# Performance work log

Measured on AMD Instinct MI355X. Metric: run time of the kernel, lower is better.

The kernel has to match this reference:

```python
import jax, jax.numpy as jnp
import numpy as np

B, T, C, H = 2, 2048, 1024, 16
NS, NL, STEP = 3, 1, 8            # n_s_token, n_l_token, online_step
NPF = NS + NL                      # tokens per frame
CHUNK = STEP * NPF                 # online chunk size = 32
D = C // H


def _build_causal_mask():
    # Faithful port of the buffer construction in __init__ (host-side numpy).
    m = np.tril(np.ones((T, T), dtype=np.float32))
    step = np.zeros((T, T), dtype=np.float32)
    for i in range(0, T, CHUNK):
        step[i:i + CHUNK, i:i + CHUNK] = 1.0
        for j in range(i, i + CHUNK, NPF):
            m[j + NS:j + NPF, :] = 0.0
            m[:, j + NS:j + NPF] = 0.0
    return jnp.asarray(((m + step) == 0.0))[None, None]  # (1,1,T,T) bool


def setup_inputs() -> dict:
    key = jax.random.key(0)
    ks = jax.random.split(key, 10)
    sc = 0.02
    return {
        "x": jax.random.normal(ks[0], (B, T, C), dtype=jnp.float32),
        "dynamic_mask": jax.random.randint(ks[1], (B, 1, T, T), 0, 2).astype(bool),
        "causal_mask": _build_causal_mask(),
        "Wq": jax.random.normal(ks[2], (C, C), dtype=jnp.float32) * sc,
        "bq": jnp.zeros((C,), dtype=jnp.float32),
        "Wk": jax.random.normal(ks[3], (C, C), dtype=jnp.float32) * sc,
        "bk": jnp.zeros((C,), dtype=jnp.float32),
        "Wv": jax.random.normal(ks[4], (C, C), dtype=jnp.float32) * sc,
        "bv": jnp.zeros((C,), dtype=jnp.float32),
        "Wo": jax.random.normal(ks[5], (C, C), dtype=jnp.float32) * sc,
        "bo": jnp.zeros((C,), dtype=jnp.float32),
    }


def reference(x, dynamic_mask, causal_mask, Wq, bq, Wk, bk, Wv, bv, Wo, bo):
    Bb, Tt, Cc = x.shape
    scale = jnp.asarray(D, x.dtype) ** -0.5
    # nn.Linear: y = x @ W.T + b ; split heads -> (B,H,T,D)
    q = (x @ Wq.T + bq).reshape(Bb, Tt, H, D).transpose(0, 2, 1, 3)
    k = (x @ Wk.T + bk).reshape(Bb, Tt, H, D).transpose(0, 2, 1, 3)
    v = (x @ Wv.T + bv).reshape(Bb, Tt, H, D).transpose(0, 2, 1, 3)
    att = jnp.einsum('bhqd,bhkd->bhqk', q, k) * scale       # (B,H,T,T)
    neg_inf = jnp.asarray(-jnp.inf, att.dtype)
    att = jnp.where(causal_mask, neg_inf, att)
    att = jnp.where(dynamic_mask, neg_inf, att)
    att = jax.nn.softmax(att, axis=-1)                      # attn_drop is identity (eval)
    y = jnp.einsum('bhqk,bhkd->bhqd', att, v)
    y = y.transpose(0, 2, 1, 3).reshape(Bb, Tt, Cc)
    return y @ Wo.T + bo                                    # resid_drop is identity (eval)
```

## Files before the change

kernel.cpp:

```cpp
#include <hip/hip_runtime.h>

#define TSEQ 2048
#define NHEAD 16
#define DHEAD 64
#define CDIM 1024
#define BATCH 2

typedef __attribute__((ext_vector_type(8))) short bfx8;
typedef __attribute__((ext_vector_type(4))) short bfx4;
typedef __attribute__((ext_vector_type(4))) float f32x4;

__device__ __forceinline__ unsigned short f2bf(float f) {
  unsigned u = __builtin_bit_cast(unsigned, f);
  u += 0x7fffu + ((u >> 16) & 1u);
  return (unsigned short)(u >> 16);
}

__device__ __forceinline__ unsigned cvtpk(float lo, float hi) {
  unsigned r;
  asm("v_cvt_pk_bf16_f32 %0, %1, %2" : "=v"(r) : "v"(lo), "v"(hi));
  return r;
}

__device__ __forceinline__ float max3f(float a, float b, float c) {
  float d;
  asm("v_max3_f32 %0, %1, %2, %3" : "=v"(d) : "v"(a), "v"(b), "v"(c));
  return d;
}

__device__ __forceinline__ void gload16(const void* g, void* l) {
  __builtin_amdgcn_global_load_lds(
      (const __attribute__((address_space(1))) unsigned*)g,
      (__attribute__((address_space(3))) unsigned*)l, 16, 0, 0);
}

__global__ __launch_bounds__(256) void convert_all(
    const float* __restrict__ x,
    const float* __restrict__ wq, const float* __restrict__ wk,
    const float* __restrict__ wv, const float* __restrict__ wo,
    short* __restrict__ xb, short* __restrict__ wall) {
  const int y = blockIdx.y;
  const float* src;
  short* dst;
  int n;
  if (y == 0) { src = x; dst = xb; n = (BATCH * TSEQ * CDIM) / 4; }
  else {
    src = (y == 1) ? wq : (y == 2) ? wk : (y == 3) ? wv : wo;
    dst = wall + (size_t)(y - 1) * CDIM * CDIM;
    n = (CDIM * CDIM) / 4;
  }
  const int i = blockIdx.x * 256 + threadIdx.x;
  if (i < n) {
    const float4 v = ((const float4*)src)[i];
    bfx4 o;
    o[0] = (short)f2bf(v.x); o[1] = (short)f2bf(v.y);
    o[2] = (short)f2bf(v.z); o[3] = (short)f2bf(v.w);
    ((bfx4*)dst)[i] = o;
  }
}

__global__ __launch_bounds__(256) void maskpack(
    const unsigned char* __restrict__ dyn,
    const unsigned char* __restrict__ causal,
    unsigned long long* __restrict__ pm) {
  const bool mbyte = (causal[32] != 0);
  const int wave = threadIdx.x >> 6, lane = threadIdx.x & 63;
  const int gid = blockIdx.x * 4 + wave;
  const int tile = gid & 31;
  const int q = (gid >> 5) & (TSEQ - 1);
  const int b = gid >> 16;
  const int g = lane >> 4, blk = (lane >> 2) & 3, r = lane & 3;
  const int k = tile * 64 + blk * 16 + g * 4 + r;
  const size_t off = ((size_t)b * TSEQ + q) * TSEQ + k;
  const bool dm = mbyte ? (dyn[off] != 0) : (((const int*)dyn)[off] != 0);
  const bool qok = (q & 3) != 3;
  const bool al =
      (((k >> 5) == (q >> 5)) || ((k <= q) && qok && (r != 3))) && !dm;
  const unsigned long long bal = __ballot(!al);
  if (lane == 0) pm[gid] = bal;
}

template <int MODE>
__global__ __launch_bounds__(256) void gemm_nt(
    const short* __restrict__ A, const short* __restrict__ Ball,
    const float* __restrict__ bias0, const float* __restrict__ bias1,
    const float* __restrict__ bias2,
    short* __restrict__ Oq, short* __restrict__ Ok, short* __restrict__ Ov,
    float* __restrict__ Of) {
  __shared__ char arena[34816];
  const int tid = threadIdx.x;
  const int w = tid >> 6, lane = tid & 63;
  const int lq = lane & 15, g = lane >> 4;
  const int wr = w >> 1, wc = w & 1;
  const int m0 = blockIdx.x * 128, n0 = blockIdx.y * 128;
  const int which = (MODE == 0) ? (int)blockIdx.z : 3;
  const short* B = Ball + (size_t)which * CDIM * CDIM;
#define ASB(bi) ((short*)(arena + (bi) * 8192))
#define BSB(bi) ((short*)(arena + 16384 + (bi) * 8192))
#define GS(bi, kt)                                                             \
  {                                                                            \
    _Pragma("unroll") for (int ph = 0; ph < 2; ++ph) {                         \
      const int c = ph * 256 + tid;                                            \
      gload16(A + (size_t)(m0 + (c >> 2)) * CDIM + (kt) * 32 + (c & 3) * 8,    \
              ASB(bi) + (ph * 256 + w * 64) * 8);                              \
      gload16(B + (size_t)(n0 + (c >> 2)) * CDIM + (kt) * 32 + (c & 3) * 8,    \
              BSB(bi) + (ph * 256 + w * 64) * 8);                              \
    }                                                                          \
  }
  GS(0, 0);
  __syncthreads();
  f32x4 acc[4][4] = {};
  for (int kt = 0; kt < CDIM / 32; ++kt) {
    const int bi = kt & 1;
    if (kt + 1 < CDIM / 32) GS(bi ^ 1, kt + 1);
    bfx8 af[4], bfr[4];
#pragma unroll
    for (int i = 0; i < 4; ++i)
      af[i] = *(const bfx8*)&ASB(bi)[(wr * 64 + i * 16 + lq) * 32 + g * 8];
#pragma unroll
    for (int i = 0; i < 4; ++i)
      bfr[i] = *(const bfx8*)&BSB(bi)[(wc * 64 + i * 16 + lq) * 32 + g * 8];
#pragma unroll
    for (int i = 0; i < 4; ++i)
#pragma unroll
      for (int j = 0; j < 4; ++j)
        acc[i][j] = __builtin_amdgcn_mfma_f32_16x16x32_bf16(af[i], bfr[j],
                                                            acc[i][j], 0, 0, 0);
    __syncthreads();
  }
#undef GS
  if (MODE == 0) {
    const float* bias = (which == 0) ? bias0 : (which == 1) ? bias1 : bias2;
    const float scale = (which == 0) ? 0.18033688011112042f : 1.0f;
    short* O = (which == 0) ? Oq : (which == 1) ? Ok : Ov;
    short* tile = (short*)arena;
#pragma unroll
    for (int i = 0; i < 4; ++i)
#pragma unroll
      for (int j = 0; j < 4; ++j) {
        const int col = wc * 64 + j * 16 + lq;
        const float bb = bias[n0 + col];
#pragma unroll
        for (int r = 0; r < 4; ++r) {
          const int row = wr * 64 + i * 16 + g * 4 + r;
          tile[row * 136 + col] = (short)f2bf((acc[i][j][r] + bb) * scale);
        }
      }
    __syncthreads();
#pragma unroll
    for (int it = 0; it < 8; ++it) {
      const int id = it * 256 + tid;
      const int m = id >> 4, c16 = id & 15;
      const int row = m0 + m;
      const int b_ = row >> 11, t = row & (TSEQ - 1);
      const int h = (n0 >> 6) + (c16 >> 3), d0 = (c16 & 7) * 8;
      *(bfx8*)&O[(((size_t)b_ * NHEAD + h) * TSEQ + t) * DHEAD + d0] =
          *(const bfx8*)&tile[m * 136 + c16 * 8];
    }
  } else {
    const float* bias = bias0;
#pragma unroll
    for (int i = 0; i < 4; ++i)
#pragma unroll
      for (int j = 0; j < 4; ++j) {
        const int col = n0 + wc * 64 + j * 16 + lq;
        const float bb = bias[col];
#pragma unroll
        for (int r = 0; r < 4; ++r) {
          const int row = m0 + wr * 64 + i * 16 + g * 4 + r;
          Of[(size_t)row * CDIM + col] = acc[i][j][r] + bb;
        }
      }
  }
}

__global__ __launch_bounds__(256) void vtrans(const short* __restrict__ V,
                                              short* __restrict__ VT) {
  __shared__ short tile[64][72];
  const int bh = blockIdx.y;
  const int t0 = blockIdx.x * 64;
  const int tid = threadIdx.x;
  const short* src = V + ((size_t)bh * TSEQ + t0) * DHEAD;
#pragma unroll
  for (int ph = 0; ph < 4; ++ph) {
    const int c = ph * 256 + tid;
    const int row = c >> 4, col = (c & 15) * 4;
    *(bfx4*)&tile[row][col] = *(const bfx4*)(src + row * DHEAD + col);
  }
  __syncthreads();
  short* dst = VT + (size_t)bh * DHEAD * TSEQ + t0;
#pragma unroll
  for (int ph = 0; ph < 4; ++ph) {
    const int c = ph * 256 + tid;
    const int d = c >> 4, tc = (c & 15) * 4;
    bfx4 o;
    o[0] = tile[tc][d]; o[1] = tile[tc + 1][d];
    o[2] = tile[tc + 2][d]; o[3] = tile[tc + 3][d];
    *(bfx4*)(dst + (size_t)d * TSEQ + tc) = o;
  }
}

struct QPhase {
  bfx8 qf0, qf1;
  f32x4 acc[4];
  float m, l;
  const unsigned short* pmr;
};

__device__ __forceinline__ void attn_half(QPhase& S, const char* kbuf,
                                          const char* vbuf, short* Pw, int t,
                                          int hf, int sw, int lq, int g) {
  const unsigned mb = (S.pmr[t << 2] >> (hf * 8)) & 0xffu;
  f32x4 st[2] = {};
  __builtin_amdgcn_s_setprio(1);
#pragma unroll
  for (int b2 = 0; b2 < 2; ++b2) {
    const int rowb = ((hf * 2 + b2) * 16 + lq) * 128;
    const bfx8 kf0 = *(const bfx8*)&kbuf[rowb + ((g * 16) ^ sw)];
    const bfx8 kf1 = *(const bfx8*)&kbuf[rowb + ((64 + g * 16) ^ sw)];
    st[b2] =
        __builtin_amdgcn_mfma_f32_16x16x32_bf16(kf0, S.qf0, st[b2], 0, 0, 0);
    st[b2] =
        __builtin_amdgcn_mfma_f32_16x16x32_bf16(kf1, S.qf1, st[b2], 0, 0, 0);
  }
  __builtin_amdgcn_s_setprio(0);
  float s8[8];
#pragma unroll
  for (int idx = 0; idx < 8; ++idx)
    s8[idx] = ((mb >> idx) & 1u) ? -3.0e38f : st[idx >> 2][idx & 3];
  const float t0 = max3f(s8[0], s8[1], s8[2]);
  const float t1 = max3f(s8[3], s8[4], s8[5]);
  const float pmax = max3f(t0, t1, fmaxf(s8[6], s8[7]));
  if (!__all(pmax - S.m <= 8.f)) {
    float smax = fmaxf(pmax, __shfl_xor(pmax, 16));
    smax = fmaxf(smax, __shfl_xor(smax, 32));
    const float mnew = fmaxf(S.m, smax);
    const float fac = __builtin_amdgcn_exp2f(S.m - mnew);
    S.l *= fac;
    float fr[4];
#pragma unroll
    for (int r = 0; r < 4; ++r) fr[r] = __shfl(fac, g * 4 + r);
#pragma unroll
    for (int dc = 0; dc < 4; ++dc) {
      S.acc[dc][0] *= fr[0]; S.acc[dc][1] *= fr[1];
      S.acc[dc][2] *= fr[2]; S.acc[dc][3] *= fr[3];
    }
    S.m = mnew;
  }
  float psum = 0.f;
#pragma unroll
  for (int idx = 0; idx < 8; ++idx) {
    const float e = __builtin_amdgcn_exp2f(s8[idx] - S.m);
    s8[idx] = e;
    psum += e;
  }
  S.l += psum;
#pragma unroll
  for (int b2 = 0; b2 < 2; ++b2) {
    uint2 u;
    u.x = cvtpk(s8[b2 * 4 + 0], s8[b2 * 4 + 1]);
    u.y = cvtpk(s8[b2 * 4 + 2], s8[b2 * 4 + 3]);
    *(uint2*)&Pw[lq * 40 + b2 * 16 + g * 4] = u;
  }
  __builtin_amdgcn_wave_barrier();
  const bfx8 pa = *(const bfx8*)&Pw[lq * 40 + g * 8];
  __builtin_amdgcn_wave_barrier();
  __builtin_amdgcn_s_setprio(1);
#pragma unroll
  for (int dc = 0; dc < 4; ++dc) {
    const bfx8 vf = *(const bfx8*)&vbuf[(dc * 16 + lq) * 128 +
                                        ((hf * 64 + g * 16) ^ sw)];
    S.acc[dc] =
        __builtin_amdgcn_mfma_f32_16x16x32_bf16(pa, vf, S.acc[dc], 0, 0, 0);
  }
  __builtin_amdgcn_s_setprio(0);
}

__global__ __launch_bounds__(512, 4) void attn(
    const short* __restrict__ Q, const short* __restrict__ K,
    const short* __restrict__ VT, const unsigned short* __restrict__ pm,
    short* __restrict__ Y) {
  __shared__ char arena[53248];
  const int tid = threadIdx.x;
  const int w = tid >> 6, lane = tid & 63;
  const int hf = w >> 2, ws = w & 3;
  const int lq = lane & 15, g = lane >> 4;
  const int bh = blockIdx.y, b = bh >> 4, h = bh & 15;
  const int tlo = blockIdx.x, thi = 31 - tlo;
  const short* Qb = Q + (size_t)bh * TSEQ * DHEAD;
  const short* Kb = K + (size_t)bh * TSEQ * DHEAD;
  const short* Vb = VT + (size_t)bh * DHEAD * TSEQ;

  QPhase lo, hi;
  {
    const int qlo = tlo * 64 + ws * 16 + lq;
    const int qhi = thi * 64 + ws * 16 + lq;
    lo.qf0 = *(const bfx8*)(Qb + (size_t)qlo * DHEAD + g * 8);
    lo.qf1 = *(const bfx8*)(Qb + (size_t)qlo * DHEAD + 32 + g * 8);
    hi.qf0 = *(const bfx8*)(Qb + (size_t)qhi * DHEAD + g * 8);
    hi.qf1 = *(const bfx8*)(Qb + (size_t)qhi * DHEAD + 32 + g * 8);
#pragma unroll
    for (int dc = 0; dc < 4; ++dc) { lo.acc[dc] = f32x4{}; hi.acc[dc] = f32x4{}; }
    lo.m = -1e30f; lo.l = 0.f; hi.m = -1e30f; hi.l = 0.f;
    lo.pmr = pm + ((size_t)(b * TSEQ + qlo) << 7) + g;
    hi.pmr = pm + ((size_t)(b * TSEQ + qhi) << 7) + g;
  }

  const int sl = lane >> 3, sc = lane & 7;
  const int ssw = (sc ^ sl) * 8;
  const int sw = (lq & 7) << 4;
  short* Pw = (short*)(arena + 32768 + w * 1280);
  short* P2w = (short*)(arena + 43008 + w * 1280);

#define STAGE(bufn, k0s)                                                      \
  {                                                                           \
    gload16(Kb + (size_t)((k0s) + w * 8 + sl) * DHEAD + ssw,                  \
            arena + (bufn) * 16384 + w * 1024);                               \
    gload16(Vb + (size_t)(w * 8 + sl) * TSEQ + (k0s) + ssw,                   \
            arena + (bufn) * 16384 + 8192 + w * 1024);                        \
  }

  STAGE(0, 0);
  __syncthreads();

  for (int t = 0; t <= thi; ++t) {
    const int buf = t & 1;
    if (t < thi) STAGE(buf ^ 1, (t + 1) * 64);
    const char* kbuf = arena + buf * 16384;
    const char* vbuf = kbuf + 8192;
    attn_half(hi, kbuf, vbuf, Pw, t, hf, sw, lq, g);
    if (t <= tlo) attn_half(lo, kbuf, vbuf, P2w, t, hf, sw, lq, g);
    __syncthreads();
  }
#undef STAGE

  float* exA = (float*)arena;
  float2* exM = (float2*)(arena + 32768);
  if (hf == 1) {
#pragma unroll
    for (int ph = 0; ph < 2; ++ph) {
      QPhase& S = ph ? hi : lo;
      float* a = exA + (ws * 2 + ph) * 1024;
#pragma unroll
      for (int dc = 0; dc < 4; ++dc)
        *(f32x4*)&a[lane * 16 + dc * 4] = S.acc[dc];
      exM[(ws * 2 + ph) * 64 + lane] = float2{S.m, S.l};
    }
  }
  __syncthreads();
  if (hf == 0) {
#pragma unroll
    for (int ph = 0; ph < 2; ++ph) {
      QPhase& S = ph ? hi : lo;
      const float* a = exA + (ws * 2 + ph) * 1024;
      const float2 mlB = exM[(ws * 2 + ph) * 64 + lane];
      const float ms = fmaxf(S.m, mlB.x);
      const float fA = __builtin_amdgcn_exp2f(S.m - ms);
      const float fB = __builtin_amdgcn_exp2f(mlB.x - ms);
      float lr = S.l * fA + mlB.y * fB;
      lr += __shfl_xor(lr, 16);
      lr += __shfl_xor(lr, 32);
      float frA[4], frB[4], li[4];
#pragma unroll
      for (int r = 0; r < 4; ++r) {
        frA[r] = __shfl(fA, g * 4 + r);
        frB[r] = __shfl(fB, g * 4 + r);
        const float lv = __shfl(lr, g * 4 + r);
        li[r] = lv > 0.f ? 1.f / lv : 0.f;
      }
      const int q0 = (ph ? thi : tlo) * 64 + ws * 16;
#pragma unroll
      for (int dc = 0; dc < 4; ++dc) {
        const f32x4 ab = *(const f32x4*)&a[lane * 16 + dc * 4];
#pragma unroll
        for (int r = 0; r < 4; ++r) {
          const int t = q0 + g * 4 + r;
          Y[((size_t)b * TSEQ + t) * CDIM + h * DHEAD + dc * 16 + lq] =
              (short)f2bf((S.acc[dc][r] * frA[r] + ab[r] * frB[r]) * li[r]);
        }
      }
    }
  }
}

extern "C" void kernel_launch(void* const* d_in, const int* in_sizes, int n_in,
                              void* d_out, int out_size, void* d_ws,
                              size_t ws_size, hipStream_t stream) {
  const float* x = (const float*)d_in[0];
  const unsigned char* dyn = (const unsigned char*)d_in[1];
  const unsigned char* causal = (const unsigned char*)d_in[2];
  const float* Wq = (const float*)d_in[3];
  const float* bq = (const float*)d_in[4];
  const float* Wk = (const float*)d_in[5];
  const float* bk = (const float*)d_in[6];
  const float* Wv = (const float*)d_in[7];
  const float* bv = (const float*)d_in[8];
  const float* Wo = (const float*)d_in[9];
  const float* bo = (const float*)d_in[10];

  char* ws = (char*)d_ws;
  const size_t MB8 = 8ull * 1024 * 1024;
  short* xb = (short*)(ws + 0 * MB8);
  short* wall = (short*)(ws + 1 * MB8);
  short* Qb = (short*)(ws + 2 * MB8);
  short* Kb = (short*)(ws + 3 * MB8);
  short* Vb = (short*)(ws + 4 * MB8);
  short* VTb = (short*)(ws + 5 * MB8);
  short* Yb = (short*)(ws + 6 * MB8);
  unsigned long long* pmask = (unsigned long long*)(ws + 7 * MB8);

  convert_all<<<dim3(4096, 5), 256, 0, stream>>>(x, Wq, Wk, Wv, Wo, xb, wall);
  maskpack<<<dim3(32768), 256, 0, stream>>>(dyn, causal, pmask);
  gemm_nt<0><<<dim3(32, 8, 3), 256, 0, stream>>>(xb, wall, bq, bk, bv, Qb, Kb,
                                                 Vb, nullptr);
  vtrans<<<dim3(32, 32), 256, 0, stream>>>(Vb, VTb);
  attn<<<dim3(16, 32), 512, 0, stream>>>(Qb, Kb, VTb,
                                         (const unsigned short*)pmask, Yb);
  gemm_nt<1><<<dim3(32, 8, 1), 256, 0, stream>>>(Yb, wall, bo, nullptr, nullptr,
                                                 nullptr, nullptr, nullptr,
                                                 (float*)d_out);
}
```

Baseline: 137.9 us.

## Fuse V transpose into QKV GEMM, retile output GEMM, share attention P buffer

The QKV projection epilogue now writes V directly in transposed layout through a padded LDS tile, which removes the separate vtrans kernel launch and its read/write pass over V. The output projection becomes its own kernel with 64-row tiles, doubling the grid to 512 blocks to fill more CUs. The attention kernel reuses one P scratch buffer for both query halves, cutting LDS use and possibly allowing more resident blocks. Risks include bank conflicts in the strided transpose reads and a hazard on the shared P buffer between the two halves.

```diff
diff --git a/kernel.cpp b/kernel.cpp
--- a/kernel.cpp
+++ b/kernel.cpp
@@ -80,20 +80,18 @@
   if (lane == 0) pm[gid] = bal;
 }
 
-template <int MODE>
-__global__ __launch_bounds__(256) void gemm_nt(
+__global__ __launch_bounds__(256) void gemm_qkv(
     const short* __restrict__ A, const short* __restrict__ Ball,
     const float* __restrict__ bias0, const float* __restrict__ bias1,
     const float* __restrict__ bias2,
-    short* __restrict__ Oq, short* __restrict__ Ok, short* __restrict__ Ov,
-    float* __restrict__ Of) {
-  __shared__ char arena[34816];
+    short* __restrict__ Oq, short* __restrict__ Ok, short* __restrict__ VT) {
+  __shared__ char arena[35072];
   const int tid = threadIdx.x;
   const int w = tid >> 6, lane = tid & 63;
   const int lq = lane & 15, g = lane >> 4;
   const int wr = w >> 1, wc = w & 1;
   const int m0 = blockIdx.x * 128, n0 = blockIdx.y * 128;
-  const int which = (MODE == 0) ? (int)blockIdx.z : 3;
+  const int which = blockIdx.z;
   const short* B = Ball + (size_t)which * CDIM * CDIM;
 #define ASB(bi) ((short*)(arena + (bi) * 8192))
 #define BSB(bi) ((short*)(arena + 16384 + (bi) * 8192))
@@ -129,75 +127,106 @@
     __syncthreads();
   }
 #undef GS
-  if (MODE == 0) {
-    const float* bias = (which == 0) ? bias0 : (which == 1) ? bias1 : bias2;
-    const float scale = (which == 0) ? 0.18033688011112042f : 1.0f;
-    short* O = (which == 0) ? Oq : (which == 1) ? Ok : Ov;
-    short* tile = (short*)arena;
-#pragma unroll
-    for (int i = 0; i < 4; ++i)
-#pragma unroll
-      for (int j = 0; j < 4; ++j) {
-        const int col = wc * 64 + j * 16 + lq;
-        const float bb = bias[n0 + col];
-#pragma unroll
-        for (int r = 0; r < 4; ++r) {
-          const int row = wr * 64 + i * 16 + g * 4 + r;
-          tile[row * 136 + col] = (short)f2bf((acc[i][j][r] + bb) * scale);
-        }
+  const float* bias = (which == 0) ? bias0 : (which == 1) ? bias1 : bias2;
+  const float scale = (which == 0) ? 0.18033688011112042f : 1.0f;
+  short* tile = (short*)arena;
+  const int rs = (which == 2) ? 137 : 136;
+#pragma unroll
+  for (int i = 0; i < 4; ++i)
+#pragma unroll
+    for (int j = 0; j < 4; ++j) {
+      const int col = wc * 64 + j * 16 + lq;
+      const float bb = bias[n0 + col];
+#pragma unroll
+      for (int r = 0; r < 4; ++r) {
+        const int row = wr * 64 + i * 16 + g * 4 + r;
+        tile[row * rs + col] = (short)f2bf((acc[i][j][r] + bb) * scale);
       }
-    __syncthreads();
+    }
+  __syncthreads();
+  const int b_ = m0 >> 11, t0 = m0 & (TSEQ - 1);
+  if (which == 2) {
+#pragma unroll
+    for (int it = 0; it < 8; ++it) {
+      const int id = it * 256 + tid;
+      const int tseg = id & 15, d128 = id >> 4;
+      const int h = (n0 >> 6) + (d128 >> 6), d = d128 & 63;
+      bfx8 o;
+#pragma unroll
+      for (int j = 0; j < 8; ++j) o[j] = tile[(tseg * 8 + j) * 137 + d128];
+      *(bfx8*)&VT[(((size_t)b_ * NHEAD + h) * DHEAD + d) * TSEQ + t0 +
+                  tseg * 8] = o;
+    }
+  } else {
+    short* O = (which == 0) ? Oq : Ok;
 #pragma unroll
     for (int it = 0; it < 8; ++it) {
       const int id = it * 256 + tid;
       const int m = id >> 4, c16 = id & 15;
-      const int row = m0 + m;
-      const int b_ = row >> 11, t = row & (TSEQ - 1);
       const int h = (n0 >> 6) + (c16 >> 3), d0 = (c16 & 7) * 8;
-      *(bfx8*)&O[(((size_t)b_ * NHEAD + h) * TSEQ + t) * DHEAD + d0] =
+      *(bfx8*)&O[(((size_t)b_ * NHEAD + h) * TSEQ + t0 + m) * DHEAD + d0] =
           *(const bfx8*)&tile[m * 136 + c16 * 8];
     }
-  } else {
-    const float* bias = bias0;
-#pragma unroll
-    for (int i = 0; i < 4; ++i)
-#pragma unroll
-      for (int j = 0; j < 4; ++j) {
-        const int col = n0 + wc * 64 + j * 16 + lq;
-        const float bb = bias[col];
-#pragma unroll
-        for (int r = 0; r < 4; ++r) {
-          const int row = m0 + wr * 64 + i * 16 + g * 4 + r;
-          Of[(size_t)row * CDIM + col] = acc[i][j][r] + bb;
-        }
+  }
+}
+
+__global__ __launch_bounds__(256) void gemm_out(
+    const short* __restrict__ A, const short* __restrict__ B,
+    const float* __restrict__ bias, float* __restrict__ Of) {
+  __shared__ char arena[24576];
+  const int tid = threadIdx.x;
+  const int w = tid >> 6, lane = tid & 63;
+  const int lq = lane & 15, g = lane >> 4;
+  const int wr = w >> 1, wc = w & 1;
+  const int m0 = blockIdx.x * 64, n0 = blockIdx.y * 128;
+#define ASB(bi) ((short*)(arena + (bi) * 4096))
+#define BSB(bi) ((short*)(arena + 8192 + (bi) * 8192))
+#define GS(bi, kt)                                                             \
+  {                                                                            \
+    gload16(A + (size_t)(m0 + (tid >> 2)) * CDIM + (kt) * 32 + (tid & 3) * 8,  \
+            ASB(bi) + (w * 64) * 8);                                           \
+    _Pragma("unroll") for (int ph = 0; ph < 2; ++ph) {                         \
+      const int c = ph * 256 + tid;                                            \
+      gload16(B + (size_t)(n0 + (c >> 2)) * CDIM + (kt) * 32 + (c & 3) * 8,    \
+              BSB(bi) + (ph * 256 + w * 64) * 8);                              \
+    }                                                                          \
+  }
+  GS(0, 0);
+  __syncthreads();
+  f32x4 acc[2][4] = {};
+  for (int kt = 0; kt < CDIM / 32; ++kt) {
+    const int bi = kt & 1;
+    if (kt + 1 < CDIM / 32) GS(bi ^ 1, kt + 1);
+    bfx8 af[2], bfr[4];
+#pragma unroll
+    for (int i = 0; i < 2; ++i)
+      af[i] = *(const bfx8*)&ASB(bi)[(wr * 32 + i * 16 + lq) * 32 + g * 8];
+#pragma unroll
+    for (int j = 0; j < 4; ++j)
+      bfr[j] = *(const bfx8*)&BSB(bi)[(wc * 64 + j * 16 + lq) * 32 + g * 8];
+#pragma unroll
+    for (int i = 0; i < 2; ++i)
+#pragma unroll
+      for (int j = 0; j < 4; ++j)
+        acc[i][j] = __builtin_amdgcn_mfma_f32_16x16x32_bf16(af[i], bfr[j],
+                                                            acc[i][j], 0, 0, 0);
+    __syncthreads();
+  }
+#undef GS
+#undef ASB
+#undef BSB
+#pragma unroll
+  for (int i = 0; i < 2; ++i)
+#pragma unroll
+    for (int j = 0; j < 4; ++j) {
+      const int col = n0 + wc * 64 + j * 16 + lq;
+      const float bb = bias[col];
+#pragma unroll
+      for (int r = 0; r < 4; ++r) {
+        const int row = m0 + wr * 32 + i * 16 + g * 4 + r;
+        Of[(size_t)row * CDIM + col] = acc[i][j][r] + bb;
       }
-  }
-}
-
-__global__ __launch_bounds__(256) void vtrans(const short* __restrict__ V,
-                                              short* __restrict__ VT) {
-  __shared__ short tile[64][72];
-  const int bh = blockIdx.y;
-  const int t0 = blockIdx.x * 64;
-  const int tid = threadIdx.x;
-  const short* src = V + ((size_t)bh * TSEQ + t0) * DHEAD;
-#pragma unroll
-  for (int ph = 0; ph < 4; ++ph) {
-    const int c = ph * 256 + tid;
-    const int row = c >> 4, col = (c & 15) * 4;
-    *(bfx4*)&tile[row][col] = *(const bfx4*)(src + row * DHEAD + col);
-  }
-  __syncthreads();
-  short* dst = VT + (size_t)bh * DHEAD * TSEQ + t0;
-#pragma unroll
-  for (int ph = 0; ph < 4; ++ph) {
-    const int c = ph * 256 + tid;
-    const int d = c >> 4, tc = (c & 15) * 4;
-    bfx4 o;
-    o[0] = tile[tc][d]; o[1] = tile[tc + 1][d];
-    o[2] = tile[tc + 2][d]; o[3] = tile[tc + 3][d];
-    *(bfx4*)(dst + (size_t)d * TSEQ + tc) = o;
-  }
+    }
 }
 
 struct QPhase {
@@ -280,7 +309,7 @@
     const short* __restrict__ Q, const short* __restrict__ K,
     const short* __restrict__ VT, const unsigned short* __restrict__ pm,
     short* __restrict__ Y) {
-  __shared__ char arena[53248];
+  __shared__ char arena[43008];
   const int tid = threadIdx.x;
   const int w = tid >> 6, lane = tid & 63;
   const int hf = w >> 2, ws = w & 3;
@@ -310,7 +339,6 @@
   const int ssw = (sc ^ sl) * 8;
   const int sw = (lq & 7) << 4;
   short* Pw = (short*)(arena + 32768 + w * 1280);
-  short* P2w = (short*)(arena + 43008 + w * 1280);
 
 #define STAGE(bufn, k0s)                                                      \
   {                                                                           \
@@ -329,7 +357,7 @@
     const char* kbuf = arena + buf * 16384;
     const char* vbuf = kbuf + 8192;
     attn_half(hi, kbuf, vbuf, Pw, t, hf, sw, lq, g);
-    if (t <= tlo) attn_half(lo, kbuf, vbuf, P2w, t, hf, sw, lq, g);
+    if (t <= tlo) attn_half(lo, kbuf, vbuf, Pw, t, hf, sw, lq, g);
     __syncthreads();
   }
 #undef STAGE
@@ -404,19 +432,16 @@
   short* wall = (short*)(ws + 1 * MB8);
   short* Qb = (short*)(ws + 2 * MB8);
   short* Kb = (short*)(ws + 3 * MB8);
-  short* Vb = (short*)(ws + 4 * MB8);
   short* VTb = (short*)(ws + 5 * MB8);
   short* Yb = (short*)(ws + 6 * MB8);
   unsigned long long* pmask = (unsigned long long*)(ws + 7 * MB8);
 
   convert_all<<<dim3(4096, 5), 256, 0, stream>>>(x, Wq, Wk, Wv, Wo, xb, wall);
   maskpack<<<dim3(32768), 256, 0, stream>>>(dyn, causal, pmask);
-  gemm_nt<0><<<dim3(32, 8, 3), 256, 0, stream>>>(xb, wall, bq, bk, bv, Qb, Kb,
-                                                 Vb, nullptr);
-  vtrans<<<dim3(32, 32), 256, 0, stream>>>(Vb, VTb);
+  gemm_qkv<<<dim3(32, 8, 3), 256, 0, stream>>>(xb, wall, bq, bk, bv, Qb, Kb,
+                                               VTb);
   attn<<<dim3(16, 32), 512, 0, stream>>>(Qb, Kb, VTb,
                                          (const unsigned short*)pmask, Yb);
-  gemm_nt<1><<<dim3(32, 8, 1), 256, 0, stream>>>(Yb, wall, bo, nullptr, nullptr,
-                                                 nullptr, nullptr, nullptr,
-                                                 (float*)d_out);
-}
+  gemm_out<<<dim3(64, 8), 256, 0, stream>>>(Yb, wall + 3 * CDIM * CDIM, bo,
+                                            (float*)d_out);
+}
```

Result: faster. 131.9 us (-4.3%).
